# Kernel tuning notes

Hardware: AMD Instinct MI355X
Metric: run time of the kernel (lower is better)

Reference implementation:

```python
import jax, jax.numpy as jnp
import numpy as np

NUM_BUCKETS = 63  # clipped 1D relative positions: clip(j-i, -31, 31) + 31


def _rp_bucket(N):
    rel = jnp.arange(N)[None, :] - jnp.arange(N)[:, None]  # j - i
    half = NUM_BUCKETS // 2
    return (jnp.clip(rel, -half, half) + half).astype(jnp.int32)  # [N, N]


def setup_inputs() -> dict:
    key = jax.random.key(0)
    ks = jax.random.split(key, 7)
    B, N, C, H = 4, 1024, 1024, 16
    hd = C // H
    g = lambda k, shp, sc: jax.random.normal(k, shp, jnp.float32) * sc
    return {
        "x": g(ks[0], (B, N, C), 1.0),
        "w_qkv": g(ks[1], (3 * C, C), C ** -0.5),   # torch Linear weight [out, in]
        "w_proj": g(ks[2], (C, C), C ** -0.5),
        "b_proj": jnp.zeros((C,), jnp.float32),
        "rpe_q_table": g(ks[3], (H, hd, NUM_BUCKETS), 0.02),
        "rpe_k_table": g(ks[4], (H, hd, NUM_BUCKETS), 0.02),
        "rpe_v_table": g(ks[5], (H, NUM_BUCKETS, hd), 0.02),
    }


def reference(x, w_qkv, w_proj, b_proj, rpe_q_table, rpe_k_table, rpe_v_table):
    B, N, C = x.shape
    H = rpe_k_table.shape[0]
    hd = C // H
    scale = hd ** -0.5

    qkv = (x @ w_qkv.T).reshape(B, N, 3, H, hd).transpose(2, 0, 3, 1, 4)  # [3,B,H,N,hd]
    q, k, v = qkv[0] * scale, qkv[1], qkv[2]

    attn = jnp.einsum('bhid,bhjd->bhij', q, k)  # [B,H,N,N]

    rp = _rp_bucket(N)            # [N,N] int32 (static w.r.t. jit)
    idx = rp[None, None]          # [1,1,N,N]

    # rpe_k(q): contextual product, transposed=True -> bias added to scores
    qL = jnp.einsum('bhid,hdm->bhim', q, rpe_k_table)           # [B,H,N,nb]
    attn = attn + jnp.take_along_axis(qL, idx, axis=-1)

    # rpe_q(k * scale).transpose(2,3)
    kL = jnp.einsum('bhjd,hdm->bhjm', k * scale, rpe_q_table)   # [B,H,N,nb]
    attn = attn + jnp.swapaxes(jnp.take_along_axis(kL, idx, axis=-1), 2, 3)

    attn = jax.nn.softmax(attn, axis=-1)

    out = jnp.einsum('bhij,bhjd->bhid', attn, v)  # [B,H,N,hd]

    # rpe_v(attn): out[b,h,i,d] += sum_j attn[b,h,i,j] * Lv[h, rp[i,j], d]
    # segment-sum attn over buckets per query row, then contract with table.
    a_t = attn.transpose(2, 3, 0, 1)  # [Ni, Nj, B, H]
    S = jax.vmap(lambda a, seg: jax.ops.segment_sum(a, seg, num_segments=NUM_BUCKETS))(a_t, rp)  # [Ni,nb,B,H]
    out = out + jnp.einsum('inbh,hnd->bhid', S, rpe_v_table)

    x_out = out.transpose(0, 2, 1, 3).reshape(B, N, C)
    return x_out @ w_proj.T + b_proj
```

## Files before the change

### kernel.cpp

```cpp
#include <hip/hip_runtime.h>

typedef unsigned short u16;
typedef __attribute__((ext_vector_type(8))) short bf16x8;
typedef __attribute__((ext_vector_type(8))) unsigned short u16x8;
typedef __attribute__((ext_vector_type(4))) float f32x4;

#define MFMA16(a, b, c) __builtin_amdgcn_mfma_f32_16x16x32_bf16(a, b, c, 0, 0, 0)

__device__ __forceinline__ u16 f2bf(float f) {
  union { float f; unsigned u; } v; v.f = f;
  unsigned r = v.u + 0x7fffu + ((v.u >> 16) & 1u);
  return (u16)(r >> 16);
}
__device__ __forceinline__ float bf2f(u16 h) {
  union { unsigned u; float f; } v; v.u = ((unsigned)h) << 16;
  return v.f;
}
__device__ __forceinline__ void gl_lds16(const u16* g, u16* l) {
  __builtin_amdgcn_global_load_lds(
      (const __attribute__((address_space(1))) unsigned int*)g,
      (__attribute__((address_space(3))) unsigned int*)l, 16, 0, 0);
}

__global__ __launch_bounds__(256) void cvt_bf16_k(
    const float* __restrict__ x, const float* __restrict__ wq,
    const float* __restrict__ wp, u16* __restrict__ xb,
    u16* __restrict__ wqb, u16* __restrict__ wpb) {
  const size_t i = (size_t)blockIdx.x * 256 + threadIdx.x;
  const float* src; u16* dst; size_t off;
  if (i < 524288)       { src = x;  dst = xb;  off = i; }
  else if (i < 917504)  { src = wq; dst = wqb; off = i - 524288; }
  else                  { src = wp; dst = wpb; off = i - 917504; }
  const f32x4 a = ((const f32x4*)src)[off * 2];
  const f32x4 b = ((const f32x4*)src)[off * 2 + 1];
  u16x8 p;
#pragma unroll
  for (int e = 0; e < 4; ++e) { p[e] = f2bf(a[e]); p[e + 4] = f2bf(b[e]); }
  ((u16x8*)dst)[off] = p;
}

__global__ __launch_bounds__(256) void qkv_gemm_mfma(
    const u16* __restrict__ xb, const u16* __restrict__ wb,
    u16* __restrict__ qb, u16* __restrict__ kb, u16* __restrict__ vb) {
  __shared__ u16 At[128 * 64];
  __shared__ u16 Bt[128 * 64];
  const int tid = threadIdx.x;
  const int lin = blockIdx.y * 24 + blockIdx.x;
  const int swz = (lin & 7) * 96 + (lin >> 3);
  const int m0 = (swz / 24) * 128;
  const int o0 = (swz % 24) * 128;
  const int l = tid & 63, wv = tid >> 6;
  const int wm = (wv >> 1) * 64, wn = (wv & 1) * 64;
  const int lr = l & 15, lg = l >> 4;
  const int srow = l >> 3, scol = (l & 7) * 8;

  f32x4 acc[4][4];
#pragma unroll
  for (int i = 0; i < 4; ++i)
#pragma unroll
    for (int j = 0; j < 4; ++j) acc[i][j] = (f32x4){0.f, 0.f, 0.f, 0.f};

  for (int k0 = 0; k0 < 1024; k0 += 64) {
#pragma unroll
    for (int ii = 0; ii < 4; ++ii) {
      const int rbase = wv * 32 + ii * 8;
      gl_lds16(xb + (size_t)(m0 + rbase + srow) * 1024 + k0 + scol, At + rbase * 64);
      gl_lds16(wb + (size_t)(o0 + rbase + srow) * 1024 + k0 + scol, Bt + rbase * 64);
    }
    __syncthreads();
#pragma unroll
    for (int kg = 0; kg < 2; ++kg) {
      const int kbyte = (kg * 32 + 8 * lg) * 2;
      bf16x8 af[4], bfr[4];
#pragma unroll
      for (int mi = 0; mi < 4; ++mi)
        af[mi] = *(const bf16x8*)((const char*)At + (wm + mi * 16 + lr) * 128 + kbyte);
#pragma unroll
      for (int ni = 0; ni < 4; ++ni)
        bfr[ni] = *(const bf16x8*)((const char*)Bt + (wn + ni * 16 + lr) * 128 + kbyte);
#pragma unroll
      for (int mi = 0; mi < 4; ++mi)
#pragma unroll
        for (int ni = 0; ni < 4; ++ni)
          acc[mi][ni] = MFMA16(af[mi], bfr[ni], acc[mi][ni]);
    }
    __syncthreads();
  }

  const int o_base = o0 + wn;
  const int which = o_base >> 10;
  const int h = (o_base >> 6) & 15;
#pragma unroll
  for (int mi = 0; mi < 4; ++mi) {
#pragma unroll
    for (int ni = 0; ni < 4; ++ni) {
      const int d = ni * 16 + lr;
#pragma unroll
      for (int r = 0; r < 4; ++r) {
        int m = m0 + wm + mi * 16 + 4 * lg + r;
        int b_ = m >> 10, n_ = m & 1023;
        size_t dst = (((size_t)(b_ * 16 + h) * 1024) + n_) * 64 + d;
        float val = acc[mi][ni][r];
        if (which == 0)      qb[dst] = f2bf(val * 0.125f);
        else if (which == 1) kb[dst] = f2bf(val);
        else                 vb[dst] = f2bf(val);
      }
    }
  }
}

__global__ __launch_bounds__(256) void vtrans_k(const u16* __restrict__ vb,
                                                u16* __restrict__ vt) {
  __shared__ u16 ts[64][72];
  const int bh = blockIdx.x >> 4;
  const int nt = (blockIdx.x & 15) * 64;
  const int t = threadIdx.x;
#pragma unroll
  for (int i = 0; i < 2; ++i) {
    int c = t * 2 + i, n = c >> 3, c8 = (c & 7) * 8;
    *(u16x8*)&ts[n][c8] = *(const u16x8*)&vb[((size_t)bh * 1024 + nt + n) * 64 + c8];
  }
  __syncthreads();
#pragma unroll
  for (int i = 0; i < 2; ++i) {
    int c = t * 2 + i, d = c >> 3, n8 = (c & 7) * 8;
    u16x8 p;
#pragma unroll
    for (int j = 0; j < 8; ++j) p[j] = ts[n8 + j][d];
    *(u16x8*)&vt[((size_t)bh * 64 + d) * 1024 + nt + n8] = p;
  }
}

__global__ __launch_bounds__(256) void rpe_proj_k(
    const u16* __restrict__ q, const u16* __restrict__ k,
    const float* __restrict__ tq, const float* __restrict__ tk,
    u16* __restrict__ qL, u16* __restrict__ kL,
    u16* __restrict__ kL0, u16* __restrict__ kL62) {
  __shared__ float tqs[64 * 63], tks[64 * 63];
  __shared__ u16 qr[16 * 64], kr[16 * 64];
  const int tid = threadIdx.x;
  const int r0 = blockIdx.x * 16;
  const int h = (r0 >> 10) & 15;
  for (int i = tid; i < 1008; i += 256) {
    ((f32x4*)tqs)[i] = ((const f32x4*)(tq + (size_t)h * 4032))[i];
    ((f32x4*)tks)[i] = ((const f32x4*)(tk + (size_t)h * 4032))[i];
  }
  for (int i = tid; i < 128; i += 256) {
    ((u16x8*)qr)[i] = ((const u16x8*)(q + (size_t)r0 * 64))[i];
    ((u16x8*)kr)[i] = ((const u16x8*)(k + (size_t)r0 * 64))[i];
  }
  __syncthreads();
  const int wv = tid >> 6, t = tid & 63;
  if (t < 63) {
#pragma unroll
    for (int rr = 0; rr < 4; ++rr) {
      const int row = wv * 4 + rr;
      float aq = 0.f, ak = 0.f;
#pragma unroll 8
      for (int d = 0; d < 64; ++d) {
        aq += bf2f(qr[row * 64 + d]) * tks[d * 63 + t];
        ak += bf2f(kr[row * 64 + d]) * tqs[d * 63 + t];
      }
      ak *= 0.125f;
      qL[(size_t)(r0 + row) * 63 + t] = f2bf(aq);
      kL[(size_t)(r0 + row) * 63 + t] = f2bf(ak);
      if (t == 0)  kL0[r0 + row] = f2bf(ak);
      if (t == 62) kL62[r0 + row] = f2bf(ak);
    }
  }
}

__global__ __launch_bounds__(512, 4) void attn_mfma_k(
    const u16* __restrict__ qg, const u16* __restrict__ kgl,
    const u16* __restrict__ vtg, const u16* __restrict__ qLg,
    const u16* __restrict__ kLg, const u16* __restrict__ kL0g,
    const u16* __restrict__ kL62g, const float* __restrict__ tvg,
    u16* __restrict__ ao) {
  __shared__ u16 Kt[64 * 64];
  __shared__ u16 Vt[64 * 64];
  __shared__ u16 Pl[8 * 16 * 64];
  __shared__ u16 qLs[128 * 63];
  __shared__ u16 kLs[64 * 63];
  __shared__ u16 segs[128 * 63];
  __shared__ u16 kl0t[64], kl62t[64];

  const int tid = threadIdx.x;
  const int raw = blockIdx.x;
  const int bid = (raw & 7) * 64 + (raw >> 3);
  const int it = bid & 7;
  const int bh = bid >> 3;
  const int h = bh & 15;
  const int b_ = bh >> 4;
  const int i0 = it * 128;
  const int l = tid & 63, wv = tid >> 6;
  const int lr = l & 15, lg = l >> 4;
  const int iw0 = i0 + wv * 16;
  const size_t gbase = (size_t)bh * 1024;

  for (int i = tid; i < 1008; i += 512) {
    ((u16x8*)segs)[i] = (u16x8){0, 0, 0, 0, 0, 0, 0, 0};
    ((u16x8*)qLs)[i] = ((const u16x8*)(qLg + (gbase + i0) * 63))[i];
  }
  bf16x8 qa[2];
  {
    const u16* qrow = qg + (gbase + iw0 + lr) * 64 + 8 * lg;
    qa[0] = *(const bf16x8*)(qrow);
    qa[1] = *(const bf16x8*)(qrow + 32);
  }
  const int st_row = tid >> 3, st_ch = tid & 7;
  const int dstb = st_row * 128 + ((st_ch * 16) ^ ((st_row & 7) << 4));
  u16x8 Kr, Vr, kLr, klr;
  {
    Kr = *(const u16x8*)(kgl + (gbase + st_row) * 64 + st_ch * 8);
    Vr = *(const u16x8*)(vtg + ((size_t)bh * 64 + st_row) * 1024 + st_ch * 8);
    *(u16x8*)((char*)Kt + dstb) = Kr;
    *(u16x8*)((char*)Vt + dstb) = Vr;
    if (i0 == 0 && tid < 504)
      ((u16x8*)kLs)[tid] = ((const u16x8*)(kLg + gbase * 63))[tid];
    if (tid < 8)       ((u16x8*)kl0t)[tid] = ((const u16x8*)(kL0g + gbase))[tid];
    else if (tid < 16) ((u16x8*)kl62t)[tid - 8] = ((const u16x8*)(kL62g + gbase))[tid - 8];
  }
  __syncthreads();

  float qL0r[4], qL62r[4];
#pragma unroll
  for (int r = 0; r < 4; ++r) {
    const int ir = wv * 16 + 4 * lg + r;
    qL0r[r] = bf2f(qLs[ir * 63 + 0]);
    qL62r[r] = bf2f(qLs[ir * 63 + 62]);
  }

  f32x4 pv[4];
#pragma unroll
  for (int db = 0; db < 4; ++db) pv[db] = (f32x4){0.f, 0.f, 0.f, 0.f};
  float lacc[4] = {0.f, 0.f, 0.f, 0.f}, racc[4] = {0.f, 0.f, 0.f, 0.f},
        rs[4] = {0.f, 0.f, 0.f, 0.f};

  for (int jt = 0; jt < 16; ++jt) {
    const int j0 = jt * 64;
    const int j0n = j0 + 64;
    const bool havenext = (jt < 15);
    const bool nband = havenext && (j0n >= i0 - 94) && (j0n <= i0 + 158);
    if (havenext) {
      Kr = *(const u16x8*)(kgl + (gbase + j0n + st_row) * 64 + st_ch * 8);
      Vr = *(const u16x8*)(vtg + ((size_t)bh * 64 + st_row) * 1024 + j0n + st_ch * 8);
      if (nband && tid < 504)
        kLr = ((const u16x8*)(kLg + (gbase + j0n) * 63))[tid];
      if (tid < 8)       klr = ((const u16x8*)(kL0g + gbase + j0n))[tid];
      else if (tid < 16) klr = ((const u16x8*)(kL62g + gbase + j0n))[tid - 8];
    }

#pragma unroll
    for (int cb = 0; cb < 4; ++cb) {
      f32x4 sc = (f32x4){0.f, 0.f, 0.f, 0.f};
#pragma unroll
      for (int kgi = 0; kgi < 2; ++kgi) {
        const int row = cb * 16 + lr;
        bf16x8 kf = *(const bf16x8*)((const char*)Kt + row * 128 +
                                     (((kgi * 32 + 8 * lg) * 2) ^ ((row & 7) << 4)));
        sc = MFMA16(qa[kgi], kf, sc);
      }
      const int jlo = j0 + cb * 16;
      const int jcol = jlo + lr;
      const int jloc = cb * 16 + lr;
      const int pcolb = jloc * 2;
      if (jlo + 15 <= iw0 - 31) {
        const float kl62 = bf2f(kl62t[jloc]);
#pragma unroll
        for (int r = 0; r < 4; ++r) {
          const float e = __expf(sc[r] + qL0r[r] + kl62);
          lacc[r] += e; rs[r] += e;
          const int prow = 4 * lg + r;
          *(u16*)((char*)Pl + wv * 2048 + prow * 128 + (pcolb ^ ((prow & 7) << 4))) = f2bf(e);
        }
      } else if (jlo >= iw0 + 46) {
        const float kl0 = bf2f(kl0t[jloc]);
#pragma unroll
        for (int r = 0; r < 4; ++r) {
          const float e = __expf(sc[r] + qL62r[r] + kl0);
          racc[r] += e; rs[r] += e;
          const int prow = 4 * lg + r;
          *(u16*)((char*)Pl + wv * 2048 + prow * 128 + (pcolb ^ ((prow & 7) << 4))) = f2bf(e);
        }
      } else {
#pragma unroll
        for (int r = 0; r < 4; ++r) {
          const int irow = iw0 + 4 * lg + r;
          int rel = jcol - irow;
          rel = rel < -31 ? -31 : (rel > 31 ? 31 : rel);
          const int m = rel + 31;
          const float bias = bf2f(qLs[(irow - i0) * 63 + m]) +
                             bf2f(kLs[jloc * 63 + 62 - m]);
          const float e = __expf(sc[r] + bias);
          rs[r] += e;
          if (m == 0)       lacc[r] += e;
          else if (m == 62) racc[r] += e;
          else              segs[(irow - i0) * 63 + m] = f2bf(e);
          const int prow = 4 * lg + r;
          *(u16*)((char*)Pl + wv * 2048 + prow * 128 + (pcolb ^ ((prow & 7) << 4))) = f2bf(e);
        }
      }
    }
#pragma unroll
    for (int db = 0; db < 4; ++db) {
#pragma unroll
      for (int kgi = 0; kgi < 2; ++kgi) {
        bf16x8 pa = *(const bf16x8*)((const char*)Pl + wv * 2048 + lr * 128 +
                                     (((kgi * 32 + 8 * lg) * 2) ^ ((lr & 7) << 4)));
        const int vrow = db * 16 + lr;
        bf16x8 vf = *(const bf16x8*)((const char*)Vt + vrow * 128 +
                                     (((kgi * 32 + 8 * lg) * 2) ^ ((vrow & 7) << 4)));
        pv[db] = MFMA16(pa, vf, pv[db]);
      }
    }
    __syncthreads();
    if (havenext) {
      *(u16x8*)((char*)Kt + dstb) = Kr;
      *(u16x8*)((char*)Vt + dstb) = Vr;
      if (nband && tid < 504) ((u16x8*)kLs)[tid] = kLr;
      if (tid < 8)       ((u16x8*)kl0t)[tid] = klr;
      else if (tid < 16) ((u16x8*)kl62t)[tid - 8] = klr;
    }
    __syncthreads();
  }

#pragma unroll
  for (int r = 0; r < 4; ++r) {
#pragma unroll
    for (int m = 1; m < 16; m <<= 1) {
      rs[r] += __shfl_xor(rs[r], m);
      lacc[r] += __shfl_xor(lacc[r], m);
      racc[r] += __shfl_xor(racc[r], m);
    }
  }
  if (lr == 0) {
#pragma unroll
    for (int r = 0; r < 4; ++r) {
      const int ir = wv * 16 + 4 * lg + r;
      segs[ir * 63 + 0] = f2bf(lacc[r]);
      segs[ir * 63 + 62] = f2bf(racc[r]);
    }
  }
  __syncthreads();

#pragma unroll
  for (int db = 0; db < 4; ++db) {
    const int d = db * 16 + lr;
    float sadd[4] = {0.f, 0.f, 0.f, 0.f};
    for (int m = 0; m < 63; ++m) {
      const float tvv = tvg[((size_t)h * 63 + m) * 64 + d];
#pragma unroll
      for (int r = 0; r < 4; ++r)
        sadd[r] += bf2f(segs[(wv * 16 + 4 * lg + r) * 63 + m]) * tvv;
    }
#pragma unroll
    for (int r = 0; r < 4; ++r) {
      const int irow = i0 + wv * 16 + 4 * lg + r;
      const float val = (pv[db][r] + sadd[r]) / rs[r];
      ao[((size_t)(b_ * 1024) + irow) * 1024 + h * 64 + d] = f2bf(val);
    }
  }
}

__global__ __launch_bounds__(256) void proj_gemm_mfma(
    const u16* __restrict__ a, const u16* __restrict__ wpb,
    const float* __restrict__ bias, float* __restrict__ out) {
  __shared__ u16 At[128 * 64];
  __shared__ u16 Bt[128 * 64];
  const int tid = threadIdx.x;
  const int m0 = blockIdx.y * 128;
  const int o0 = blockIdx.x * 128;
  const int l = tid & 63, wv = tid >> 6;
  const int wm = (wv >> 1) * 64, wn = (wv & 1) * 64;
  const int lr = l & 15, lg = l >> 4;
  const int srow = l >> 3, scol = (l & 7) * 8;

  f32x4 acc[4][4];
#pragma unroll
  for (int i = 0; i < 4; ++i)
#pragma unroll
    for (int j = 0; j < 4; ++j) acc[i][j] = (f32x4){0.f, 0.f, 0.f, 0.f};

  for (int k0 = 0; k0 < 1024; k0 += 64) {
#pragma unroll
    for (int ii = 0; ii < 4; ++ii) {
      const int rbase = wv * 32 + ii * 8;
      gl_lds16(a + (size_t)(m0 + rbase + srow) * 1024 + k0 + scol, At + rbase * 64);
      gl_lds16(wpb + (size_t)(o0 + rbase + srow) * 1024 + k0 + scol, Bt + rbase * 64);
    }
    __syncthreads();
#pragma unroll
    for (int kg = 0; kg < 2; ++kg) {
      const int kbyte = (kg * 32 + 8 * lg) * 2;
      bf16x8 af[4], bfr[4];
#pragma unroll
      for (int mi = 0; mi < 4; ++mi)
        af[mi] = *(const bf16x8*)((const char*)At + (wm + mi * 16 + lr) * 128 + kbyte);
#pragma unroll
      for (int ni = 0; ni < 4; ++ni)
        bfr[ni] = *(const bf16x8*)((const char*)Bt + (wn + ni * 16 + lr) * 128 + kbyte);
#pragma unroll
      for (int mi = 0; mi < 4; ++mi)
#pragma unroll
        for (int ni = 0; ni < 4; ++ni)
          acc[mi][ni] = MFMA16(af[mi], bfr[ni], acc[mi][ni]);
    }
    __syncthreads();
  }
#pragma unroll
  for (int mi = 0; mi < 4; ++mi) {
#pragma unroll
    for (int ni = 0; ni < 4; ++ni) {
      const int o = o0 + wn + ni * 16 + lr;
      const float bv = bias[o];
#pragma unroll
      for (int r = 0; r < 4; ++r) {
        const int m = m0 + wm + mi * 16 + 4 * lg + r;
        out[(size_t)m * 1024 + o] = acc[mi][ni][r] + bv;
      }
    }
  }
}

extern "C" void kernel_launch(void* const* d_in, const int* in_sizes, int n_in,
                              void* d_out, int out_size, void* d_ws, size_t ws_size,
                              hipStream_t stream) {
  const float* x      = (const float*)d_in[0];
  const float* w_qkv  = (const float*)d_in[1];
  const float* w_proj = (const float*)d_in[2];
  const float* b_proj = (const float*)d_in[3];
  const float* tq     = (const float*)d_in[4];
  const float* tk     = (const float*)d_in[5];
  const float* tv     = (const float*)d_in[6];
  float* out = (float*)d_out;

  char* w8 = (char*)d_ws;
  u16* qb   = (u16*)(w8);
  u16* kb   = (u16*)(w8 + (8ull << 20));
  u16* vb   = (u16*)(w8 + (16ull << 20));
  u16* vt   = (u16*)(w8 + (24ull << 20));
  u16* aob  = (u16*)(w8 + (32ull << 20));
  u16* qL   = (u16*)(w8 + (40ull << 20));
  u16* kL   = (u16*)(w8 + (49ull << 20));
  u16* kL0  = (u16*)(w8 + (58ull << 20));
  u16* kL62 = (u16*)(w8 + (59ull << 20));
  u16* xb   = (u16*)(w8 + (60ull << 20));
  u16* wqb  = (u16*)(w8 + (68ull << 20));
  u16* wpb  = (u16*)(w8 + (74ull << 20));

  hipLaunchKernelGGL(cvt_bf16_k, dim3(4096), dim3(256), 0, stream,
                     x, w_qkv, w_proj, xb, wqb, wpb);
  hipLaunchKernelGGL(qkv_gemm_mfma, dim3(24, 32), dim3(256), 0, stream,
                     xb, wqb, qb, kb, vb);
  hipLaunchKernelGGL(vtrans_k, dim3(1024), dim3(256), 0, stream, vb, vt);
  hipLaunchKernelGGL(rpe_proj_k, dim3(4096), dim3(256), 0, stream,
                     qb, kb, tq, tk, qL, kL, kL0, kL62);
  hipLaunchKernelGGL(attn_mfma_k, dim3(512), dim3(512), 0, stream,
                     qb, kb, vt, qL, kL, kL0, kL62, tv, aob);
  hipLaunchKernelGGL(proj_gemm_mfma, dim3(8, 32), dim3(256), 0, stream,
                     aob, wpb, b_proj, out);
}
```

Baseline: 328.9 us.

## Keep softmax probabilities in registers by transposing the QK MFMA and shuffling

The QK^T MFMA now has its operands swapped, so each lane holds scores for a single query row across four key columns. The exp'd probabilities are packed to bf16 pairs and rearranged with cross-lane shuffles into the A-operand layout of the PV MFMA, which removes the per-wave LDS scratch buffer Pl and its scattered stores and loads. Row sums become scalars per lane and need fewer reductions, at the cost of extra shuffles per tile. The bf16 conversion also moves to a cheaper round-half-up packing that is not round-to-nearest-even.

```diff
diff --git a/kernel.cpp b/kernel.cpp
--- a/kernel.cpp
+++ b/kernel.cpp
@@ -3,6 +3,7 @@
 typedef unsigned short u16;
 typedef __attribute__((ext_vector_type(8))) short bf16x8;
 typedef __attribute__((ext_vector_type(8))) unsigned short u16x8;
+typedef __attribute__((ext_vector_type(4))) unsigned short u16x4;
 typedef __attribute__((ext_vector_type(4))) float f32x4;
 
 #define MFMA16(a, b, c) __builtin_amdgcn_mfma_f32_16x16x32_bf16(a, b, c, 0, 0, 0)
@@ -15,6 +16,10 @@
 __device__ __forceinline__ float bf2f(u16 h) {
   union { unsigned u; float f; } v; v.u = ((unsigned)h) << 16;
   return v.f;
+}
+__device__ __forceinline__ unsigned pk2bf(float a, float b) {
+  union { float f; unsigned u; } x, y; x.f = a; y.f = b;
+  return ((x.u + 0x8000u) >> 16) | ((y.u + 0x8000u) & 0xffff0000u);
 }
 __device__ __forceinline__ void gl_lds16(const u16* g, u16* l) {
   __builtin_amdgcn_global_load_lds(
@@ -178,11 +183,10 @@
     u16* __restrict__ ao) {
   __shared__ u16 Kt[64 * 64];
   __shared__ u16 Vt[64 * 64];
-  __shared__ u16 Pl[8 * 16 * 64];
   __shared__ u16 qLs[128 * 63];
   __shared__ u16 kLs[64 * 63];
   __shared__ u16 segs[128 * 63];
-  __shared__ u16 kl0t[64], kl62t[64];
+  __shared__ u16x4 kl0t4[16], kl62t4[16];
 
   const int tid = threadIdx.x;
   const int raw = blockIdx.x;
@@ -217,24 +221,18 @@
     *(u16x8*)((char*)Vt + dstb) = Vr;
     if (i0 == 0 && tid < 504)
       ((u16x8*)kLs)[tid] = ((const u16x8*)(kLg + gbase * 63))[tid];
-    if (tid < 8)       ((u16x8*)kl0t)[tid] = ((const u16x8*)(kL0g + gbase))[tid];
-    else if (tid < 16) ((u16x8*)kl62t)[tid - 8] = ((const u16x8*)(kL62g + gbase))[tid - 8];
+    if (tid < 8)       ((u16x8*)kl0t4)[tid] = ((const u16x8*)(kL0g + gbase))[tid];
+    else if (tid < 16) ((u16x8*)kl62t4)[tid - 8] = ((const u16x8*)(kL62g + gbase))[tid - 8];
   }
   __syncthreads();
 
-  float qL0r[4], qL62r[4];
-#pragma unroll
-  for (int r = 0; r < 4; ++r) {
-    const int ir = wv * 16 + 4 * lg + r;
-    qL0r[r] = bf2f(qLs[ir * 63 + 0]);
-    qL62r[r] = bf2f(qLs[ir * 63 + 62]);
-  }
+  const float qL0v = bf2f(qLs[(wv * 16 + lr) * 63 + 0]);
+  const float qL62v = bf2f(qLs[(wv * 16 + lr) * 63 + 62]);
 
   f32x4 pv[4];
 #pragma unroll
   for (int db = 0; db < 4; ++db) pv[db] = (f32x4){0.f, 0.f, 0.f, 0.f};
-  float lacc[4] = {0.f, 0.f, 0.f, 0.f}, racc[4] = {0.f, 0.f, 0.f, 0.f},
-        rs[4] = {0.f, 0.f, 0.f, 0.f};
+  float lacc = 0.f, racc = 0.f, rs = 0.f;
 
   for (int jt = 0; jt < 16; ++jt) {
     const int j0 = jt * 64;
@@ -250,6 +248,7 @@
       else if (tid < 16) klr = ((const u16x8*)(kL62g + gbase + j0n))[tid - 8];
     }
 
+    unsigned w[4][2];
 #pragma unroll
     for (int cb = 0; cb < 4; ++cb) {
       f32x4 sc = (f32x4){0.f, 0.f, 0.f, 0.f};
@@ -258,90 +257,92 @@
         const int row = cb * 16 + lr;
         bf16x8 kf = *(const bf16x8*)((const char*)Kt + row * 128 +
                                      (((kgi * 32 + 8 * lg) * 2) ^ ((row & 7) << 4)));
-        sc = MFMA16(qa[kgi], kf, sc);
+        sc = MFMA16(kf, qa[kgi], sc);
       }
       const int jlo = j0 + cb * 16;
-      const int jcol = jlo + lr;
-      const int jloc = cb * 16 + lr;
-      const int pcolb = jloc * 2;
+      float ev[4];
       if (jlo + 15 <= iw0 - 31) {
-        const float kl62 = bf2f(kl62t[jloc]);
+        const u16x4 kv = kl62t4[cb * 4 + lg];
 #pragma unroll
         for (int r = 0; r < 4; ++r) {
-          const float e = __expf(sc[r] + qL0r[r] + kl62);
-          lacc[r] += e; rs[r] += e;
-          const int prow = 4 * lg + r;
-          *(u16*)((char*)Pl + wv * 2048 + prow * 128 + (pcolb ^ ((prow & 7) << 4))) = f2bf(e);
+          const float e = __expf(sc[r] + qL0v + bf2f(kv[r]));
+          lacc += e; rs += e; ev[r] = e;
         }
       } else if (jlo >= iw0 + 46) {
-        const float kl0 = bf2f(kl0t[jloc]);
+        const u16x4 kv = kl0t4[cb * 4 + lg];
 #pragma unroll
         for (int r = 0; r < 4; ++r) {
-          const float e = __expf(sc[r] + qL62r[r] + kl0);
-          racc[r] += e; rs[r] += e;
-          const int prow = 4 * lg + r;
-          *(u16*)((char*)Pl + wv * 2048 + prow * 128 + (pcolb ^ ((prow & 7) << 4))) = f2bf(e);
+          const float e = __expf(sc[r] + qL62v + bf2f(kv[r]));
+          racc += e; rs += e; ev[r] = e;
         }
       } else {
 #pragma unroll
         for (int r = 0; r < 4; ++r) {
-          const int irow = iw0 + 4 * lg + r;
-          int rel = jcol - irow;
+          const int jloc = cb * 16 + 4 * lg + r;
+          int rel = (j0 + jloc) - (iw0 + lr);
           rel = rel < -31 ? -31 : (rel > 31 ? 31 : rel);
           const int m = rel + 31;
-          const float bias = bf2f(qLs[(irow - i0) * 63 + m]) +
+          const float bias = bf2f(qLs[(wv * 16 + lr) * 63 + m]) +
                              bf2f(kLs[jloc * 63 + 62 - m]);
           const float e = __expf(sc[r] + bias);
-          rs[r] += e;
-          if (m == 0)       lacc[r] += e;
-          else if (m == 62) racc[r] += e;
-          else              segs[(irow - i0) * 63 + m] = f2bf(e);
-          const int prow = 4 * lg + r;
-          *(u16*)((char*)Pl + wv * 2048 + prow * 128 + (pcolb ^ ((prow & 7) << 4))) = f2bf(e);
+          rs += e;
+          if (m == 0)       lacc += e;
+          else if (m == 62) racc += e;
+          else              segs[(wv * 16 + lr) * 63 + m] = f2bf(e);
+          ev[r] = e;
         }
       }
-    }
+      w[cb][0] = pk2bf(ev[0], ev[1]);
+      w[cb][1] = pk2bf(ev[2], ev[3]);
+    }
+
+    unsigned pf0[4], pf1[4];
+#pragma unroll
+    for (int u = 0; u < 4; ++u) {
+      const int s = (l & 15) | ((((lg & 1) * 2) + (u >> 1)) << 4);
+      const unsigned a0 = (unsigned)__shfl((int)w[0][u & 1], s, 64);
+      const unsigned b0 = (unsigned)__shfl((int)w[1][u & 1], s, 64);
+      const unsigned a1 = (unsigned)__shfl((int)w[2][u & 1], s, 64);
+      const unsigned b1 = (unsigned)__shfl((int)w[3][u & 1], s, 64);
+      pf0[u] = (lg >> 1) ? b0 : a0;
+      pf1[u] = (lg >> 1) ? b1 : a1;
+    }
+    union { unsigned u[4]; bf16x8 v; } pA0, pA1;
+#pragma unroll
+    for (int u = 0; u < 4; ++u) { pA0.u[u] = pf0[u]; pA1.u[u] = pf1[u]; }
+
 #pragma unroll
     for (int db = 0; db < 4; ++db) {
-#pragma unroll
-      for (int kgi = 0; kgi < 2; ++kgi) {
-        bf16x8 pa = *(const bf16x8*)((const char*)Pl + wv * 2048 + lr * 128 +
-                                     (((kgi * 32 + 8 * lg) * 2) ^ ((lr & 7) << 4)));
-        const int vrow = db * 16 + lr;
-        bf16x8 vf = *(const bf16x8*)((const char*)Vt + vrow * 128 +
-                                     (((kgi * 32 + 8 * lg) * 2) ^ ((vrow & 7) << 4)));
-        pv[db] = MFMA16(pa, vf, pv[db]);
-      }
+      const int vrow = db * 16 + lr;
+      bf16x8 vf0 = *(const bf16x8*)((const char*)Vt + vrow * 128 +
+                                    (((8 * lg) * 2) ^ ((vrow & 7) << 4)));
+      bf16x8 vf1 = *(const bf16x8*)((const char*)Vt + vrow * 128 +
+                                    (((32 + 8 * lg) * 2) ^ ((vrow & 7) << 4)));
+      pv[db] = MFMA16(pA0.v, vf0, pv[db]);
+      pv[db] = MFMA16(pA1.v, vf1, pv[db]);
     }
     __syncthreads();
     if (havenext) {
       *(u16x8*)((char*)Kt + dstb) = Kr;
       *(u16x8*)((char*)Vt + dstb) = Vr;
       if (nband && tid < 504) ((u16x8*)kLs)[tid] = kLr;
-      if (tid < 8)       ((u16x8*)kl0t)[tid] = klr;
-      else if (tid < 16) ((u16x8*)kl62t)[tid - 8] = klr;
-    }
-    __syncthreads();
-  }
-
-#pragma unroll
-  for (int r = 0; r < 4; ++r) {
-#pragma unroll
-    for (int m = 1; m < 16; m <<= 1) {
-      rs[r] += __shfl_xor(rs[r], m);
-      lacc[r] += __shfl_xor(lacc[r], m);
-      racc[r] += __shfl_xor(racc[r], m);
-    }
-  }
-  if (lr == 0) {
-#pragma unroll
-    for (int r = 0; r < 4; ++r) {
-      const int ir = wv * 16 + 4 * lg + r;
-      segs[ir * 63 + 0] = f2bf(lacc[r]);
-      segs[ir * 63 + 62] = f2bf(racc[r]);
-    }
+      if (tid < 8)       ((u16x8*)kl0t4)[tid] = klr;
+      else if (tid < 16) ((u16x8*)kl62t4)[tid - 8] = klr;
+    }
+    __syncthreads();
+  }
+
+  rs += __shfl_xor(rs, 16); rs += __shfl_xor(rs, 32);
+  lacc += __shfl_xor(lacc, 16); lacc += __shfl_xor(lacc, 32);
+  racc += __shfl_xor(racc, 16); racc += __shfl_xor(racc, 32);
+  if (l < 16) {
+    segs[(wv * 16 + l) * 63 + 0] = f2bf(lacc);
+    segs[(wv * 16 + l) * 63 + 62] = f2bf(racc);
   }
   __syncthreads();
+  float rsr[4];
+#pragma unroll
+  for (int r = 0; r < 4; ++r) rsr[r] = __shfl(rs, 4 * lg + r, 64);
 
 #pragma unroll
   for (int db = 0; db < 4; ++db) {
@@ -356,7 +357,7 @@
 #pragma unroll
     for (int r = 0; r < 4; ++r) {
       const int irow = i0 + wv * 16 + 4 * lg + r;
-      const float val = (pv[db][r] + sadd[r]) / rs[r];
+      const float val = (pv[db][r] + sadd[r]) / rsr[r];
       ao[((size_t)(b_ * 1024) + irow) * 1024 + h * 64 + d] = f2bf(val);
     }
   }
```

After: 327.5 us. About the same (-0.4%).
